# Kernel optimization log

Hardware: AMD Instinct MI355X
Metric: run time of the kernel (lower is better)

Reference implementation:

```python
import jax, jax.numpy as jnp
import numpy as np

UNITS = 512
OUT_STEPS = 32
FEAT = 12  # Dense(12) output fed back as LSTM input


def _lstm_cell(x_t, h, c, W, U, b):
    # Keras LSTMCell gate order: i, f, c(bar), o
    z = x_t @ W + h @ U + b                     # [B, 4U]
    i, f, g, o = jnp.split(z, 4, axis=-1)
    i = jax.nn.sigmoid(i)
    f = jax.nn.sigmoid(f)
    g = jnp.tanh(g)
    o = jax.nn.sigmoid(o)
    c_new = f * c + i * g
    h_new = o * jnp.tanh(c_new)
    return h_new, c_new


def setup_inputs() -> dict:
    key = jax.random.key(0)
    ks = jax.random.split(key, 6)
    B, T = 4096, 128
    s_in = 1.0 / np.sqrt(FEAT)
    s_rec = 1.0 / np.sqrt(UNITS)
    return {
        "x":  jax.random.normal(ks[0], (B, T, FEAT), dtype=jnp.float32),
        "W":  jax.random.normal(ks[1], (FEAT, 4 * UNITS), dtype=jnp.float32) * s_in,
        "U":  jax.random.normal(ks[2], (UNITS, 4 * UNITS), dtype=jnp.float32) * s_rec,
        "b":  jnp.zeros((4 * UNITS,), dtype=jnp.float32),
        "Wd": jax.random.normal(ks[4], (UNITS, FEAT), dtype=jnp.float32) * s_rec,
        "bd": jnp.zeros((FEAT,), dtype=jnp.float32),
    }


def reference(x, W, U, b, Wd, bd):
    B = x.shape[0]
    h0 = jnp.zeros((B, UNITS), dtype=x.dtype)
    c0 = jnp.zeros((B, UNITS), dtype=x.dtype)

    # warmup: run LSTM over full input sequence, keep final state
    def warm_step(carry, x_t):
        h, c = carry
        h, c = _lstm_cell(x_t, h, c, W, U, b)
        return (h, c), None

    (h, c), _ = jax.lax.scan(warm_step, (h0, c0), jnp.swapaxes(x, 0, 1))
    pred0 = h @ Wd + bd                          # [B, 12]

    def ar_step(carry, _):
        h, c, pred = carry
        h, c = _lstm_cell(pred, h, c, W, U, b)
        pred = h @ Wd + bd
        return (h, c, pred), pred

    _, preds_rest = jax.lax.scan(ar_step, (h, c, pred0), None, length=OUT_STEPS - 1)
    preds = jnp.concatenate([pred0[None], preds_rest], axis=0)  # [out_steps, B, 12]
    return jnp.transpose(preds, (1, 0, 2))       # [B, out_steps, 12]
```

## Files before the change

kernel.cpp:

```cpp
#include <hip/hip_runtime.h>


typedef __bf16 bf16;
typedef __attribute__((ext_vector_type(8))) __bf16 bf16x8;
typedef __attribute__((ext_vector_type(4))) float f32x4;

#define NB    4096
#define TSEQ  128
#define FEAT  12
#define UNITS 512
#define NZ    2048
#define OUTS  32

#define BM 128
#define BK 64

#define OFF_UT   ((size_t)0)
#define OFF_UTA  (OFF_UT  + (size_t)NZ*UNITS*2)
#define OFF_WT   (OFF_UTA + (size_t)NZ*UNITS*2)
#define OFF_B2   (OFF_WT  + (size_t)NZ*32*2)
#define OFF_WDT  (OFF_B2  + (size_t)NZ*4)
#define OFF_H0   (OFF_WDT + (size_t)16*UNITS*2)
#define OFF_H1   (OFF_H0  + (size_t)NB*UNITS*2)
#define OFF_C    (OFF_H1  + (size_t)NB*UNITS*2)
#define WS_NEED  (OFF_C   + (size_t)NB*UNITS*4)
#define OFF_HALL (WS_NEED)
#define HALL_SL  ((size_t)NB*UNITS)
#define WS_BIG   (OFF_HALL + (size_t)OUTS*NB*UNITS*2)

__device__ __forceinline__ float fast_exp2(float x){ return __builtin_amdgcn_exp2f(x); }
__device__ __forceinline__ float fast_rcp (float x){ return __builtin_amdgcn_rcpf(x); }
__device__ __forceinline__ float sigm_(float x){ return fast_rcp(1.f + fast_exp2(-1.4426950408889634f*x)); }
__device__ __forceinline__ float tanh_(float x){ return 1.f - 2.f*fast_rcp(1.f + fast_exp2(2.8853900817779268f*x)); }

__global__ void prep_u_kernel(const float* __restrict__ U, const float* __restrict__ W,
                              const float* __restrict__ Wd,
                              bf16* __restrict__ Ut, bf16* __restrict__ Uta){
  __shared__ float su[64][65];
  __shared__ float sa[64][65];
  const int n0 = blockIdx.x * 64;
  const int k0 = blockIdx.y * 64;
  const int tx = threadIdx.x & 63;
  const int rr = threadIdx.x >> 6;
  #pragma unroll 4
  for (int it = 0; it < 16; ++it){
    int k = it*4 + rr;
    float u = U[(size_t)(k0+k)*NZ + n0 + tx];
    float a = u;
    #pragma unroll
    for (int j = 0; j < FEAT; ++j) a += Wd[(k0+k)*FEAT + j] * W[(size_t)j*NZ + n0 + tx];
    su[tx][k] = u;
    sa[tx][k] = a;
  }
  __syncthreads();
  #pragma unroll 4
  for (int it = 0; it < 16; ++it){
    int nl = it*4 + rr;
    Ut [(size_t)(n0+nl)*UNITS + k0 + tx] = (bf16)su[nl][tx];
    Uta[(size_t)(n0+nl)*UNITS + k0 + tx] = (bf16)sa[nl][tx];
  }
}

__global__ void prep_w_kernel(const float* __restrict__ W, const float* __restrict__ b,
                              const float* __restrict__ bd, const float* __restrict__ Wd,
                              bf16* __restrict__ Wt, float* __restrict__ b2,
                              bf16* __restrict__ Wdt){
  const int n = blockIdx.x*256 + threadIdx.x;
  float acc = b[n];
  #pragma unroll
  for (int j = 0; j < FEAT; ++j){
    float w = W[(size_t)j*NZ + n];
    Wt[(size_t)n*32 + j] = (bf16)w;
    acc += bd[j] * w;
  }
  #pragma unroll
  for (int j = FEAT; j < 32; ++j) Wt[(size_t)n*32 + j] = (bf16)0.f;
  b2[n] = acc;
  if (n < UNITS){
    #pragma unroll
    for (int j = 0; j < FEAT; ++j) Wdt[(size_t)j*UNITS + n] = (bf16)Wd[(size_t)n*FEAT + j];
    #pragma unroll
    for (int j = FEAT; j < 16; ++j) Wdt[(size_t)j*UNITS + n] = (bf16)0.f;
  }
}

template<int HAS_X>
__launch_bounds__(256, 2)
__global__ void lstm_step_kernel(const bf16* __restrict__ hin, bf16* __restrict__ hout,
                                 float* __restrict__ c,
                                 const bf16* __restrict__ Bt,
                                 const float* __restrict__ bias,
                                 const float* __restrict__ xt,
                                 const bf16* __restrict__ Wt)
{
  __shared__ alignas(16) char lds[65536];

  int bid = blockIdx.x;
  bid = (bid & 7) * 64 + (bid >> 3);
  const int mt = bid >> 4;
  const int nu = bid & 15;
  const int m0 = mt * BM;

  const int tid  = threadIdx.x;
  const int lane = tid & 63;
  const int wid  = tid >> 6;
  const int wm   = wid >> 1, wn = wid & 1;
  const int l15  = lane & 15;
  const int kgrp = lane >> 4;
  const int l7   = lane & 7;
  const int l8   = lane >> 3;

  const bf16* agp = hin + (size_t)(m0 + wid*32 + l8)*UNITS + l7*8;
  const int   aoff = (wid*32 + l8)*128 + ((l7 ^ l8) << 4);
  int zcv[4];
  #pragma unroll
  for (int i = 0; i < 4; ++i){
    int lnl = wid*32 + i*8 + l8;
    zcv[i] = ((lnl & 3) << 9) + nu*32 + (lnl >> 2);
  }

  f32x4 acc[4][4];
  #pragma unroll
  for (int i = 0; i < 4; ++i)
    #pragma unroll
    for (int j = 0; j < 4; ++j) acc[i][j] = f32x4{0.f,0.f,0.f,0.f};

  bf16x8 rA[2][4], rB[2][4];

  auto load_set = [&](int s, int k0){
    #pragma unroll
    for (int i = 0; i < 4; ++i){
      rA[s][i] = *reinterpret_cast<const bf16x8*>(agp + (size_t)i*8*UNITS + k0);
      rB[s][i] = *reinterpret_cast<const bf16x8*>(Bt + (size_t)zcv[i]*UNITS + k0 + l7*8);
    }
  };
  auto write_set = [&](int s, int bi){
    char* A = lds + (bi << 14);
    char* B = lds + 32768 + (bi << 14);
    #pragma unroll
    for (int i = 0; i < 4; ++i){
      *reinterpret_cast<bf16x8*>(A + aoff + i*1024) = rA[s][i];
      *reinterpret_cast<bf16x8*>(B + aoff + i*1024) = rB[s][i];
    }
  };
  auto compute = [&](int bi){
    const char* A = lds + (bi << 14);
    const char* B = lds + 32768 + (bi << 14);
    #pragma unroll
    for (int kk = 0; kk < 2; ++kk){
      const int sa = (((kk*4 + kgrp) ^ (l15 & 7)) << 4);
      bf16x8 af[4], bq[4];
      #pragma unroll
      for (int f = 0; f < 4; ++f){
        af[f] = *reinterpret_cast<const bf16x8*>(A + (wm*64 + f*16 + l15)*128 + sa);
        bq[f] = *reinterpret_cast<const bf16x8*>(B + (wn*64 + f*16 + l15)*128 + sa);
      }
      #pragma unroll
      for (int i = 0; i < 4; ++i)
        #pragma unroll
        for (int j = 0; j < 4; ++j)
          acc[i][j] = __builtin_amdgcn_mfma_f32_16x16x32_bf16(af[i], bq[j], acc[i][j], 0, 0, 0);
    }
  };

  bf16x8 xa[4], wq[4];
  if (HAS_X){
    #pragma unroll
    for (int f = 0; f < 4; ++f){
      int row = m0 + wm*64 + f*16 + l15;
      const float* xr = xt + (size_t)row * (TSEQ*FEAT);
      bf16x8 v;
      #pragma unroll
      for (int j = 0; j < 8; ++j) v[j] = (bf16)0.f;
      if (kgrp == 0){
        float4 a = *reinterpret_cast<const float4*>(xr);
        float4 b = *reinterpret_cast<const float4*>(xr + 4);
        v[0]=(bf16)a.x; v[1]=(bf16)a.y; v[2]=(bf16)a.z; v[3]=(bf16)a.w;
        v[4]=(bf16)b.x; v[5]=(bf16)b.y; v[6]=(bf16)b.z; v[7]=(bf16)b.w;
      } else if (kgrp == 1){
        float4 a = *reinterpret_cast<const float4*>(xr + 8);
        v[0]=(bf16)a.x; v[1]=(bf16)a.y; v[2]=(bf16)a.z; v[3]=(bf16)a.w;
      }
      xa[f] = v;
      int lnl = wn*64 + f*16 + l15;
      int zc  = ((lnl & 3) << 9) + nu*32 + (lnl >> 2);
      wq[f] = *reinterpret_cast<const bf16x8*>(Wt + (size_t)zc*32 + kgrp*8);
    }
  }
  const int eu  = tid & 31;
  const int erg = tid >> 5;
  const int cu  = nu*32 + eu;
  float bi_ = bias[0*UNITS + cu];
  float bf_ = bias[1*UNITS + cu];
  float bg_ = bias[2*UNITS + cu];
  float bo_ = bias[3*UNITS + cu];

  load_set(0, 0);
  load_set(1, BK);

  const int rbase = m0 + erg*16;
  float cold[16];
  {
    const float* cp = c + (size_t)rbase*UNITS + cu;
    #pragma unroll
    for (int r = 0; r < 16; ++r) cold[r] = cp[(size_t)r*UNITS];
  }

  write_set(0, 0);
  asm volatile("s_waitcnt lgkmcnt(0)" ::: "memory");
  __builtin_amdgcn_sched_barrier(0);
  __builtin_amdgcn_s_barrier();

  #pragma unroll
  for (int t = 0; t < 8; ++t){
    const int p = t & 1;
    if (t + 2 < 8) load_set(p, (t+2)*BK);
    compute(p);
    if (t < 7){
      write_set(p ^ 1, p ^ 1);
      asm volatile("s_waitcnt lgkmcnt(0)" ::: "memory");
      __builtin_amdgcn_sched_barrier(0);
      __builtin_amdgcn_s_barrier();
    }
  }

  if (HAS_X){
    #pragma unroll
    for (int i = 0; i < 4; ++i)
      #pragma unroll
      for (int j = 0; j < 4; ++j)
        acc[i][j] = __builtin_amdgcn_mfma_f32_16x16x32_bf16(xa[i], wq[j], acc[i][j], 0, 0, 0);
  }

  asm volatile("s_waitcnt lgkmcnt(0)" ::: "memory");
  __builtin_amdgcn_sched_barrier(0);
  __builtin_amdgcn_s_barrier();

  #pragma unroll
  for (int fm = 0; fm < 4; ++fm){
    #pragma unroll
    for (int fn = 0; fn < 4; ++fn){
      int col  = wn*64 + fn*16 + l15;
      int srow = wm*16 + fm*4 + kgrp;
      *reinterpret_cast<f32x4*>(lds + col*512 + ((srow ^ (col & 7)) << 4)) = acc[fm][fn];
    }
  }
  asm volatile("s_waitcnt lgkmcnt(0)" ::: "memory");
  __builtin_amdgcn_sched_barrier(0);
  __builtin_amdgcn_s_barrier();

  #pragma unroll
  for (int q = 0; q < 4; ++q){
    const int s = erg*4 + q;
    f32x4 zi = *reinterpret_cast<const f32x4*>(lds + (eu*4+0)*512 + ((s ^ ((eu*4+0)&7)) << 4));
    f32x4 zf = *reinterpret_cast<const f32x4*>(lds + (eu*4+1)*512 + ((s ^ ((eu*4+1)&7)) << 4));
    f32x4 zg = *reinterpret_cast<const f32x4*>(lds + (eu*4+2)*512 + ((s ^ ((eu*4+2)&7)) << 4));
    f32x4 zo = *reinterpret_cast<const f32x4*>(lds + (eu*4+3)*512 + ((s ^ ((eu*4+3)&7)) << 4));
    #pragma unroll
    for (int rr = 0; rr < 4; ++rr){
      int r = q*4 + rr;
      float iv = sigm_(zi[rr] + bi_);
      float fv = sigm_(zf[rr] + bf_);
      float gv = tanh_(zg[rr] + bg_);
      float ov = sigm_(zo[rr] + bo_);
      float cn = fv*cold[r] + iv*gv;
      size_t idx = (size_t)(rbase + r)*UNITS + cu;
      c[idx]    = cn;
      hout[idx] = (bf16)(ov*tanh_(cn));
    }
  }
}

__global__ void pred_all_kernel(const bf16* __restrict__ hbase, size_t slot_stride, int s0,
                                const bf16* __restrict__ Wdt,
                                const float* __restrict__ bd, float* __restrict__ out){
  const int slot = s0 + blockIdx.y;
  const bf16* h  = hbase + (size_t)blockIdx.y * slot_stride;
  const int tid = threadIdx.x, lane = tid & 63, wid = tid >> 6;
  const int l15 = lane & 15, kg = lane >> 4;
  const int r0 = blockIdx.x*64 + wid*16;
  f32x4 acc = f32x4{0.f,0.f,0.f,0.f};
  const bf16* ap = h   + (size_t)(r0 + l15)*UNITS + kg*8;
  const bf16* bp = Wdt + (size_t)l15*UNITS + kg*8;
  #pragma unroll
  for (int ks = 0; ks < 16; ++ks){
    bf16x8 a = *reinterpret_cast<const bf16x8*>(ap + ks*32);
    bf16x8 b = *reinterpret_cast<const bf16x8*>(bp + ks*32);
    acc = __builtin_amdgcn_mfma_f32_16x16x32_bf16(a, b, acc, 0, 0, 0);
  }
  if (l15 < FEAT){
    float bdv = bd[l15];
    #pragma unroll
    for (int r = 0; r < 4; ++r){
      int row = r0 + kg*4 + r;
      out[(size_t)row*(OUTS*FEAT) + slot*FEAT + l15] = acc[r] + bdv;
    }
  }
}

extern "C" void kernel_launch(void* const* d_in, const int* in_sizes, int n_in,
                              void* d_out, int out_size, void* d_ws, size_t ws_size,
                              hipStream_t stream){
  const float* x  = (const float*)d_in[0];
  const float* W  = (const float*)d_in[1];
  const float* U  = (const float*)d_in[2];
  const float* b  = (const float*)d_in[3];
  const float* Wd = (const float*)d_in[4];
  const float* bd = (const float*)d_in[5];
  float* out = (float*)d_out;
  (void)in_sizes; (void)n_in; (void)out_size;
  if (ws_size < WS_NEED) return;
  const bool big = ws_size >= WS_BIG;

  char* ws  = (char*)d_ws;
  bf16* Ut  = (bf16*)(ws + OFF_UT);
  bf16* Uta = (bf16*)(ws + OFF_UTA);
  bf16* Wt  = (bf16*)(ws + OFF_WT);
  float* b2 = (float*)(ws + OFF_B2);
  bf16* Wdt = (bf16*)(ws + OFF_WDT);
  bf16* h0  = (bf16*)(ws + OFF_H0);
  bf16* h1  = (bf16*)(ws + OFF_H1);
  float* c  = (float*)(ws + OFF_C);
  bf16* hall= (bf16*)(ws + OFF_HALL);

  hipMemsetAsync(h0, 0, (size_t)NB*UNITS*2, stream);
  hipMemsetAsync(c,  0, (size_t)NB*UNITS*4, stream);
  prep_u_kernel<<<dim3(32, 8), 256, 0, stream>>>(U, W, Wd, Ut, Uta);
  prep_w_kernel<<<8, 256, 0, stream>>>(W, b, bd, Wd, Wt, b2, Wdt);

  if (big){
    bf16* hcur = h0; bf16* hnxt = h1;
    for (int t = 0; t < TSEQ; ++t){
      bf16* dst = (t == TSEQ-1) ? hall : hnxt;
      lstm_step_kernel<1><<<512, 256, 0, stream>>>(hcur, dst, c, Ut, b, x + t*FEAT, Wt);
      hnxt = hcur; hcur = dst;
    }
    for (int s = 1; s < OUTS; ++s)
      lstm_step_kernel<0><<<512, 256, 0, stream>>>(hall + (size_t)(s-1)*HALL_SL,
                                                   hall + (size_t)s*HALL_SL,
                                                   c, Uta, b2, nullptr, nullptr);
    pred_all_kernel<<<dim3(NB/64, OUTS), 256, 0, stream>>>(hall, HALL_SL, 0, Wdt, bd, out);
  } else {
    bf16* hcur = h0; bf16* hnxt = h1;
    for (int t = 0; t < TSEQ; ++t){
      lstm_step_kernel<1><<<512, 256, 0, stream>>>(hcur, hnxt, c, Ut, b, x + t*FEAT, Wt);
      bf16* tmp = hcur; hcur = hnxt; hnxt = tmp;
    }
    pred_all_kernel<<<dim3(NB/64, 1), 256, 0, stream>>>(hcur, 0, 0, Wdt, bd, out);
    for (int s = 1; s < OUTS; ++s){
      lstm_step_kernel<0><<<512, 256, 0, stream>>>(hcur, hnxt, c, Uta, b2, nullptr, nullptr);
      bf16* tmp = hcur; hcur = hnxt; hnxt = tmp;
      pred_all_kernel<<<dim3(NB/64, 1), 256, 0, stream>>>(hcur, 0, s, Wdt, bd, out);
    }
  }
}
```

Baseline: 2.950 ms.

## Replace per-step launches with persistent cooperative LSTM kernel using row-tile barriers

Runs all 159 recurrent steps inside one cooperative persistent kernel of 512 blocks. Each block keeps its cell state in registers instead of reading and writing c in global memory every step. Steps are synchronized with a per-row-tile atomic counter barrier rather than kernel boundaries, so only the 16 blocks sharing a batch tile wait on each other. This removes launch overhead and the c round-trip, but relies on all blocks being co-resident and adds spin-wait latency. If the cooperative launch fails, it falls back to the old multi-launch path.

```diff
diff --git a/kernel.cpp b/kernel.cpp
--- a/kernel.cpp
+++ b/kernel.cpp
@@ -11,6 +11,7 @@
 #define UNITS 512
 #define NZ    2048
 #define OUTS  32
+#define NSTEP (TSEQ + OUTS - 1)
 
 #define BM 128
 #define BK 64
@@ -23,7 +24,8 @@
 #define OFF_H0   (OFF_WDT + (size_t)16*UNITS*2)
 #define OFF_H1   (OFF_H0  + (size_t)NB*UNITS*2)
 #define OFF_C    (OFF_H1  + (size_t)NB*UNITS*2)
-#define WS_NEED  (OFF_C   + (size_t)NB*UNITS*4)
+#define OFF_BAR  (OFF_C   + (size_t)NB*UNITS*4)
+#define WS_NEED  (OFF_BAR + 4096)
 #define OFF_HALL (WS_NEED)
 #define HALL_SL  ((size_t)NB*UNITS)
 #define WS_BIG   (OFF_HALL + (size_t)OUTS*NB*UNITS*2)
@@ -84,6 +86,226 @@
   }
 }
 
+__launch_bounds__(256, 2)
+__global__ void lstm_persistent(bf16* __restrict__ hA,
+                                bf16* __restrict__ hB,
+                                bf16* __restrict__ hall,
+                                const bf16* __restrict__ Ut,
+                                const bf16* __restrict__ Uta,
+                                const float* __restrict__ b1,
+                                const float* __restrict__ b2,
+                                const float* __restrict__ x,
+                                const bf16* __restrict__ Wt,
+                                unsigned* __restrict__ bar)
+{
+  __shared__ alignas(16) char lds[65536];
+
+  int bid = blockIdx.x;
+  bid = (bid & 7) * 64 + (bid >> 3);
+  const int mt = bid >> 4;
+  const int nu = bid & 15;
+  const int m0 = mt * BM;
+
+  const int tid  = threadIdx.x;
+  const int lane = tid & 63;
+  const int wid  = tid >> 6;
+  const int wm   = wid >> 1, wn = wid & 1;
+  const int l15  = lane & 15;
+  const int kgrp = lane >> 4;
+  const int l7   = lane & 7;
+  const int l8   = lane >> 3;
+
+  const int    aoff = (wid*32 + l8)*128 + ((l7 ^ l8) << 4);
+  const size_t arow = (size_t)(m0 + wid*32 + l8)*UNITS + l7*8;
+  int zcv[4];
+  #pragma unroll
+  for (int i = 0; i < 4; ++i){
+    int lnl = wid*32 + i*8 + l8;
+    zcv[i] = ((lnl & 3) << 9) + nu*32 + (lnl >> 2);
+  }
+
+  bf16x8 wq[4];
+  int    xrow[4];
+  #pragma unroll
+  for (int f = 0; f < 4; ++f){
+    int lnl = wn*64 + f*16 + l15;
+    int zc  = ((lnl & 3) << 9) + nu*32 + (lnl >> 2);
+    wq[f] = *reinterpret_cast<const bf16x8*>(Wt + (size_t)zc*32 + kgrp*8);
+    xrow[f] = (m0 + wm*64 + f*16 + l15) * (TSEQ*FEAT);
+  }
+  const int eu  = tid & 31;
+  const int erg = tid >> 5;
+  const int cu  = nu*32 + eu;
+  const float bI1 = b1[0*UNITS+cu], bF1 = b1[1*UNITS+cu], bG1 = b1[2*UNITS+cu], bO1 = b1[3*UNITS+cu];
+  const float bI2 = b2[0*UNITS+cu], bF2 = b2[1*UNITS+cu], bG2 = b2[2*UNITS+cu], bO2 = b2[3*UNITS+cu];
+  const int rbase = m0 + erg*16;
+
+  float cc[16];
+  #pragma unroll
+  for (int r = 0; r < 16; ++r) cc[r] = 0.f;
+
+  f32x4 acc[4][4];
+  bf16x8 rA[2][4], rB[2][4];
+
+  #pragma unroll 1
+  for (int t = 0; t < NSTEP; ++t){
+    const bool hasx = (t < TSEQ);
+    const bf16* Bt = hasx ? Ut : Uta;
+    const bf16* hi = (t < TSEQ) ? ((t & 1) ? hB : hA)
+                                : hall + (size_t)(t - TSEQ)*HALL_SL;
+    bf16* ho = (t < TSEQ-1) ? ((t & 1) ? hA : hB)
+                            : hall + (size_t)(t - (TSEQ-1))*HALL_SL;
+
+    bf16x8 xa[4];
+    if (hasx){
+      #pragma unroll
+      for (int f = 0; f < 4; ++f){
+        const float* xr = x + xrow[f] + t*FEAT;
+        bf16x8 v;
+        #pragma unroll
+        for (int j = 0; j < 8; ++j) v[j] = (bf16)0.f;
+        if (kgrp == 0){
+          float4 a = *reinterpret_cast<const float4*>(xr);
+          float4 b = *reinterpret_cast<const float4*>(xr + 4);
+          v[0]=(bf16)a.x; v[1]=(bf16)a.y; v[2]=(bf16)a.z; v[3]=(bf16)a.w;
+          v[4]=(bf16)b.x; v[5]=(bf16)b.y; v[6]=(bf16)b.z; v[7]=(bf16)b.w;
+        } else if (kgrp == 1){
+          float4 a = *reinterpret_cast<const float4*>(xr + 8);
+          v[0]=(bf16)a.x; v[1]=(bf16)a.y; v[2]=(bf16)a.z; v[3]=(bf16)a.w;
+        }
+        xa[f] = v;
+      }
+    }
+
+    if (t > 0){
+      if (tid == 0){
+        const unsigned tgt = 16u * (unsigned)t;
+        while (__hip_atomic_load(&bar[mt], __ATOMIC_RELAXED, __HIP_MEMORY_SCOPE_AGENT) < tgt)
+          __builtin_amdgcn_s_sleep(4);
+        __builtin_amdgcn_fence(__ATOMIC_ACQUIRE, "agent");
+      }
+      __syncthreads();
+    }
+
+    auto load_set = [&](int s, int k0){
+      #pragma unroll
+      for (int i = 0; i < 4; ++i){
+        rA[s][i] = *reinterpret_cast<const bf16x8*>(hi + arow + (size_t)i*8*UNITS + k0);
+        rB[s][i] = *reinterpret_cast<const bf16x8*>(Bt + (size_t)zcv[i]*UNITS + k0 + l7*8);
+      }
+    };
+    auto write_set = [&](int s, int bi){
+      char* A = lds + (bi << 14);
+      char* B = lds + 32768 + (bi << 14);
+      #pragma unroll
+      for (int i = 0; i < 4; ++i){
+        *reinterpret_cast<bf16x8*>(A + aoff + i*1024) = rA[s][i];
+        *reinterpret_cast<bf16x8*>(B + aoff + i*1024) = rB[s][i];
+      }
+    };
+    auto compute = [&](int bi){
+      const char* A = lds + (bi << 14);
+      const char* B = lds + 32768 + (bi << 14);
+      #pragma unroll
+      for (int kk = 0; kk < 2; ++kk){
+        const int sa = (((kk*4 + kgrp) ^ (l15 & 7)) << 4);
+        bf16x8 af[4], bq[4];
+        #pragma unroll
+        for (int f = 0; f < 4; ++f){
+          af[f] = *reinterpret_cast<const bf16x8*>(A + (wm*64 + f*16 + l15)*128 + sa);
+          bq[f] = *reinterpret_cast<const bf16x8*>(B + (wn*64 + f*16 + l15)*128 + sa);
+        }
+        #pragma unroll
+        for (int i = 0; i < 4; ++i)
+          #pragma unroll
+          for (int j = 0; j < 4; ++j)
+            acc[i][j] = __builtin_amdgcn_mfma_f32_16x16x32_bf16(af[i], bq[j], acc[i][j], 0, 0, 0);
+      }
+    };
+
+    #pragma unroll
+    for (int i = 0; i < 4; ++i)
+      #pragma unroll
+      for (int j = 0; j < 4; ++j) acc[i][j] = f32x4{0.f,0.f,0.f,0.f};
+
+    load_set(0, 0);
+    load_set(1, BK);
+    write_set(0, 0);
+    asm volatile("s_waitcnt lgkmcnt(0)" ::: "memory");
+    __builtin_amdgcn_sched_barrier(0);
+    __builtin_amdgcn_s_barrier();
+
+    #pragma unroll
+    for (int kt = 0; kt < 8; ++kt){
+      const int p = kt & 1;
+      if (kt + 2 < 8) load_set(p, (kt+2)*BK);
+      compute(p);
+      if (kt < 7){
+        write_set(p ^ 1, p ^ 1);
+        asm volatile("s_waitcnt lgkmcnt(0)" ::: "memory");
+        __builtin_amdgcn_sched_barrier(0);
+        __builtin_amdgcn_s_barrier();
+      }
+    }
+
+    if (hasx){
+      #pragma unroll
+      for (int i = 0; i < 4; ++i)
+        #pragma unroll
+        for (int j = 0; j < 4; ++j)
+          acc[i][j] = __builtin_amdgcn_mfma_f32_16x16x32_bf16(xa[i], wq[j], acc[i][j], 0, 0, 0);
+    }
+
+    asm volatile("s_waitcnt lgkmcnt(0)" ::: "memory");
+    __builtin_amdgcn_sched_barrier(0);
+    __builtin_amdgcn_s_barrier();
+
+    #pragma unroll
+    for (int fm = 0; fm < 4; ++fm){
+      #pragma unroll
+      for (int fn = 0; fn < 4; ++fn){
+        int col  = wn*64 + fn*16 + l15;
+        int srow = wm*16 + fm*4 + kgrp;
+        *reinterpret_cast<f32x4*>(lds + col*512 + ((srow ^ (col & 7)) << 4)) = acc[fm][fn];
+      }
+    }
+    asm volatile("s_waitcnt lgkmcnt(0)" ::: "memory");
+    __builtin_amdgcn_sched_barrier(0);
+    __builtin_amdgcn_s_barrier();
+
+    const float bi_ = hasx ? bI1 : bI2;
+    const float bf_ = hasx ? bF1 : bF2;
+    const float bg_ = hasx ? bG1 : bG2;
+    const float bo_ = hasx ? bO1 : bO2;
+
+    #pragma unroll
+    for (int q = 0; q < 4; ++q){
+      const int s = erg*4 + q;
+      f32x4 zi = *reinterpret_cast<const f32x4*>(lds + (eu*4+0)*512 + ((s ^ ((eu*4+0)&7)) << 4));
+      f32x4 zf = *reinterpret_cast<const f32x4*>(lds + (eu*4+1)*512 + ((s ^ ((eu*4+1)&7)) << 4));
+      f32x4 zg = *reinterpret_cast<const f32x4*>(lds + (eu*4+2)*512 + ((s ^ ((eu*4+2)&7)) << 4));
+      f32x4 zo = *reinterpret_cast<const f32x4*>(lds + (eu*4+3)*512 + ((s ^ ((eu*4+3)&7)) << 4));
+      #pragma unroll
+      for (int rr2 = 0; rr2 < 4; ++rr2){
+        int r = q*4 + rr2;
+        float iv = sigm_(zi[rr2] + bi_);
+        float fv = sigm_(zf[rr2] + bf_);
+        float gv = tanh_(zg[rr2] + bg_);
+        float ov = sigm_(zo[rr2] + bo_);
+        float cn = fv*cc[r] + iv*gv;
+        cc[r] = cn;
+        ho[(size_t)(rbase + r)*UNITS + cu] = (bf16)(ov*tanh_(cn));
+      }
+    }
+
+    if (t < NSTEP - 1){
+      __syncthreads();
+      if (tid == 0)
+        __hip_atomic_fetch_add(&bar[mt], 1u, __ATOMIC_RELEASE, __HIP_MEMORY_SCOPE_AGENT);
+    }
+  }
+}
+
 template<int HAS_X>
 __launch_bounds__(256, 2)
 __global__ void lstm_step_kernel(const bf16* __restrict__ hin, bf16* __restrict__ hout,
@@ -94,13 +316,11 @@
                                  const bf16* __restrict__ Wt)
 {
   __shared__ alignas(16) char lds[65536];
-
   int bid = blockIdx.x;
   bid = (bid & 7) * 64 + (bid >> 3);
   const int mt = bid >> 4;
   const int nu = bid & 15;
   const int m0 = mt * BM;
-
   const int tid  = threadIdx.x;
   const int lane = tid & 63;
   const int wid  = tid >> 6;
@@ -126,7 +346,6 @@
     for (int j = 0; j < 4; ++j) acc[i][j] = f32x4{0.f,0.f,0.f,0.f};
 
   bf16x8 rA[2][4], rB[2][4];
-
   auto load_set = [&](int s, int k0){
     #pragma unroll
     for (int i = 0; i < 4; ++i){
@@ -197,7 +416,6 @@
 
   load_set(0, 0);
   load_set(1, BK);
-
   const int rbase = m0 + erg*16;
   float cold[16];
   {
@@ -205,7 +423,6 @@
     #pragma unroll
     for (int r = 0; r < 16; ++r) cold[r] = cp[(size_t)r*UNITS];
   }
-
   write_set(0, 0);
   asm volatile("s_waitcnt lgkmcnt(0)" ::: "memory");
   __builtin_amdgcn_sched_barrier(0);
@@ -235,7 +452,6 @@
   asm volatile("s_waitcnt lgkmcnt(0)" ::: "memory");
   __builtin_amdgcn_sched_barrier(0);
   __builtin_amdgcn_s_barrier();
-
   #pragma unroll
   for (int fm = 0; fm < 4; ++fm){
     #pragma unroll
@@ -321,36 +537,55 @@
   bf16* h0  = (bf16*)(ws + OFF_H0);
   bf16* h1  = (bf16*)(ws + OFF_H1);
   float* c  = (float*)(ws + OFF_C);
+  unsigned* bar = (unsigned*)(ws + OFF_BAR);
   bf16* hall= (bf16*)(ws + OFF_HALL);
 
   hipMemsetAsync(h0, 0, (size_t)NB*UNITS*2, stream);
   hipMemsetAsync(c,  0, (size_t)NB*UNITS*4, stream);
+  hipMemsetAsync(bar, 0, 4096, stream);
   prep_u_kernel<<<dim3(32, 8), 256, 0, stream>>>(U, W, Wd, Ut, Uta);
   prep_w_kernel<<<8, 256, 0, stream>>>(W, b, bd, Wd, Wt, b2, Wdt);
 
+  bool done = false;
   if (big){
-    bf16* hcur = h0; bf16* hnxt = h1;
-    for (int t = 0; t < TSEQ; ++t){
-      bf16* dst = (t == TSEQ-1) ? hall : hnxt;
-      lstm_step_kernel<1><<<512, 256, 0, stream>>>(hcur, dst, c, Ut, b, x + t*FEAT, Wt);
-      hnxt = hcur; hcur = dst;
-    }
-    for (int s = 1; s < OUTS; ++s)
-      lstm_step_kernel<0><<<512, 256, 0, stream>>>(hall + (size_t)(s-1)*HALL_SL,
-                                                   hall + (size_t)s*HALL_SL,
-                                                   c, Uta, b2, nullptr, nullptr);
-    pred_all_kernel<<<dim3(NB/64, OUTS), 256, 0, stream>>>(hall, HALL_SL, 0, Wdt, bd, out);
-  } else {
-    bf16* hcur = h0; bf16* hnxt = h1;
-    for (int t = 0; t < TSEQ; ++t){
-      lstm_step_kernel<1><<<512, 256, 0, stream>>>(hcur, hnxt, c, Ut, b, x + t*FEAT, Wt);
-      bf16* tmp = hcur; hcur = hnxt; hnxt = tmp;
-    }
-    pred_all_kernel<<<dim3(NB/64, 1), 256, 0, stream>>>(hcur, 0, 0, Wdt, bd, out);
-    for (int s = 1; s < OUTS; ++s){
-      lstm_step_kernel<0><<<512, 256, 0, stream>>>(hcur, hnxt, c, Uta, b2, nullptr, nullptr);
-      bf16* tmp = hcur; hcur = hnxt; hnxt = tmp;
-      pred_all_kernel<<<dim3(NB/64, 1), 256, 0, stream>>>(hcur, 0, s, Wdt, bd, out);
+    const float* xc = x;
+    void* args[] = { (void*)&h0, (void*)&h1, (void*)&hall,
+                     (void*)&Ut, (void*)&Uta, (void*)&b, (void*)&b2,
+                     (void*)&xc, (void*)&Wt, (void*)&bar };
+    hipError_t e = hipLaunchCooperativeKernel(
+        reinterpret_cast<void*>(lstm_persistent),
+        dim3(512), dim3(256), args, 0, stream);
+    if (e == hipSuccess){
+      pred_all_kernel<<<dim3(NB/64, OUTS), 256, 0, stream>>>(hall, HALL_SL, 0, Wdt, bd, out);
+      done = true;
+    }
+  }
+
+  if (!done){
+    if (big){
+      bf16* hcur = h0; bf16* hnxt = h1;
+      for (int t = 0; t < TSEQ; ++t){
+        bf16* dst = (t == TSEQ-1) ? hall : hnxt;
+        lstm_step_kernel<1><<<512, 256, 0, stream>>>(hcur, dst, c, Ut, b, x + t*FEAT, Wt);
+        hnxt = hcur; hcur = dst;
+      }
+      for (int s = 1; s < OUTS; ++s)
+        lstm_step_kernel<0><<<512, 256, 0, stream>>>(hall + (size_t)(s-1)*HALL_SL,
+                                                     hall + (size_t)s*HALL_SL,
+                                                     c, Uta, b2, nullptr, nullptr);
+      pred_all_kernel<<<dim3(NB/64, OUTS), 256, 0, stream>>>(hall, HALL_SL, 0, Wdt, bd, out);
+    } else {
+      bf16* hcur = h0; bf16* hnxt = h1;
+      for (int t = 0; t < TSEQ; ++t){
+        lstm_step_kernel<1><<<512, 256, 0, stream>>>(hcur, hnxt, c, Ut, b, x + t*FEAT, Wt);
+        bf16* tmp = hcur; hcur = hnxt; hnxt = tmp;
+      }
+      pred_all_kernel<<<dim3(NB/64, 1), 256, 0, stream>>>(hcur, 0, 0, Wdt, bd, out);
+      for (int s = 1; s < OUTS; ++s){
+        lstm_step_kernel<0><<<512, 256, 0, stream>>>(hcur, hnxt, c, Uta, b2, nullptr, nullptr);
+        bf16* tmp = hcur; hcur = hnxt; hnxt = tmp;
+        pred_all_kernel<<<dim3(NB/64, 1), 256, 0, stream>>>(hcur, 0, s, Wdt, bd, out);
+      }
     }
   }
 }
```

Measured after the change: 5.886 ms. +99.6%, slower.

## Pre-pack recurrent weights into MFMA fragment order and load B directly to registers

Applied to the files above, without the earlier changes.

The prep kernel now writes the transposed U and U+Wd·W matrices in a packed layout that matches each wave's MFMA B-fragment order. The step kernel loads B fragments straight from global memory into registers instead of staging them through LDS, so only the A (hidden state) tile goes through shared memory. This cuts LDS writes and reads for B and the bank traffic they cause. In exchange it needs more registers for the doubled B prefetch buffers, which may pressure occupancy under the 2-waves-per-SIMD launch bound, and each wave now fetches its own B data from global memory or L2.

```diff
diff --git a/kernel.cpp b/kernel.cpp
--- a/kernel.cpp
+++ b/kernel.cpp
@@ -33,9 +33,20 @@
 __device__ __forceinline__ float sigm_(float x){ return fast_rcp(1.f + fast_exp2(-1.4426950408889634f*x)); }
 __device__ __forceinline__ float tanh_(float x){ return 1.f - 2.f*fast_rcp(1.f + fast_exp2(2.8853900817779268f*x)); }
 
+__device__ __forceinline__ size_t bp_off(int n, int k){
+  int g  = n >> 9;
+  int uc = n & 511;
+  int nu = uc >> 5, uo = uc & 31;
+  int lnl = uo*4 + g;
+  int wn = lnl >> 6, f = (lnl >> 4) & 3, l15 = lnl & 15;
+  int it = k >> 6, kk = (k >> 5) & 1, kgrp = (k >> 3) & 3, e = k & 7;
+  int frag = (((nu*2 + wn)*4 + f)*8 + it)*2 + kk;
+  return (size_t)frag*1024 + kgrp*256 + l15*16 + e*2;
+}
+
 __global__ void prep_u_kernel(const float* __restrict__ U, const float* __restrict__ W,
                               const float* __restrict__ Wd,
-                              bf16* __restrict__ Ut, bf16* __restrict__ Uta){
+                              bf16* __restrict__ Utp, bf16* __restrict__ Utap){
   __shared__ float su[64][65];
   __shared__ float sa[64][65];
   const int n0 = blockIdx.x * 64;
@@ -53,11 +64,17 @@
     sa[tx][k] = a;
   }
   __syncthreads();
-  #pragma unroll 4
-  for (int it = 0; it < 16; ++it){
-    int nl = it*4 + rr;
-    Ut [(size_t)(n0+nl)*UNITS + k0 + tx] = (bf16)su[nl][tx];
-    Uta[(size_t)(n0+nl)*UNITS + k0 + tx] = (bf16)sa[nl][tx];
+  const int nl = threadIdx.x & 63;
+  const int q  = threadIdx.x >> 6;
+  const float (*src)[65] = (q & 1) ? sa : su;
+  char* dst = (char*)((q & 1) ? Utap : Utp);
+  const int kh = (q >> 1) * 32;
+  #pragma unroll
+  for (int kc = 0; kc < 32; kc += 8){
+    bf16x8 v;
+    #pragma unroll
+    for (int e = 0; e < 8; ++e) v[e] = (bf16)src[nl][kh + kc + e];
+    *reinterpret_cast<bf16x8*>(dst + bp_off(n0 + nl, k0 + kh + kc)) = v;
   }
 }
 
@@ -88,7 +105,7 @@
 __launch_bounds__(256, 2)
 __global__ void lstm_step_kernel(const bf16* __restrict__ hin, bf16* __restrict__ hout,
                                  float* __restrict__ c,
-                                 const bf16* __restrict__ Bt,
+                                 const bf16* __restrict__ Bp,
                                  const float* __restrict__ bias,
                                  const float* __restrict__ xt,
                                  const bf16* __restrict__ Wt)
@@ -112,12 +129,8 @@
 
   const bf16* agp = hin + (size_t)(m0 + wid*32 + l8)*UNITS + l7*8;
   const int   aoff = (wid*32 + l8)*128 + ((l7 ^ l8) << 4);
-  int zcv[4];
-  #pragma unroll
-  for (int i = 0; i < 4; ++i){
-    int lnl = wid*32 + i*8 + l8;
-    zcv[i] = ((lnl & 3) << 9) + nu*32 + (lnl >> 2);
-  }
+
+  const char* bp = (const char*)Bp + (size_t)(nu*2 + wn)*65536 + kgrp*256 + l15*16;
 
   f32x4 acc[4][4];
   #pragma unroll
@@ -125,41 +138,41 @@
     #pragma unroll
     for (int j = 0; j < 4; ++j) acc[i][j] = f32x4{0.f,0.f,0.f,0.f};
 
-  bf16x8 rA[2][4], rB[2][4];
-
-  auto load_set = [&](int s, int k0){
-    #pragma unroll
-    for (int i = 0; i < 4; ++i){
+  bf16x8 rA[2][4];
+  bf16x8 rB[2][8];
+
+  auto loadA_set = [&](int s, int k0){
+    #pragma unroll
+    for (int i = 0; i < 4; ++i)
       rA[s][i] = *reinterpret_cast<const bf16x8*>(agp + (size_t)i*8*UNITS + k0);
-      rB[s][i] = *reinterpret_cast<const bf16x8*>(Bt + (size_t)zcv[i]*UNITS + k0 + l7*8);
-    }
   };
-  auto write_set = [&](int s, int bi){
+  auto loadB_set = [&](int s, int it){
+    #pragma unroll
+    for (int f = 0; f < 4; ++f)
+      #pragma unroll
+      for (int kk = 0; kk < 2; ++kk)
+        rB[s][f*2+kk] = *reinterpret_cast<const bf16x8*>(bp + f*16384 + it*2048 + kk*1024);
+  };
+  auto writeA_set = [&](int s, int bi){
     char* A = lds + (bi << 14);
-    char* B = lds + 32768 + (bi << 14);
-    #pragma unroll
-    for (int i = 0; i < 4; ++i){
+    #pragma unroll
+    for (int i = 0; i < 4; ++i)
       *reinterpret_cast<bf16x8*>(A + aoff + i*1024) = rA[s][i];
-      *reinterpret_cast<bf16x8*>(B + aoff + i*1024) = rB[s][i];
-    }
   };
-  auto compute = [&](int bi){
+  auto compute = [&](int bi, int s){
     const char* A = lds + (bi << 14);
-    const char* B = lds + 32768 + (bi << 14);
     #pragma unroll
     for (int kk = 0; kk < 2; ++kk){
       const int sa = (((kk*4 + kgrp) ^ (l15 & 7)) << 4);
-      bf16x8 af[4], bq[4];
-      #pragma unroll
-      for (int f = 0; f < 4; ++f){
+      bf16x8 af[4];
+      #pragma unroll
+      for (int f = 0; f < 4; ++f)
         af[f] = *reinterpret_cast<const bf16x8*>(A + (wm*64 + f*16 + l15)*128 + sa);
-        bq[f] = *reinterpret_cast<const bf16x8*>(B + (wn*64 + f*16 + l15)*128 + sa);
-      }
       #pragma unroll
       for (int i = 0; i < 4; ++i)
         #pragma unroll
         for (int j = 0; j < 4; ++j)
-          acc[i][j] = __builtin_amdgcn_mfma_f32_16x16x32_bf16(af[i], bq[j], acc[i][j], 0, 0, 0);
+          acc[i][j] = __builtin_amdgcn_mfma_f32_16x16x32_bf16(af[i], rB[s][j*2+kk], acc[i][j], 0, 0, 0);
     }
   };
 
@@ -195,8 +208,10 @@
   float bg_ = bias[2*UNITS + cu];
   float bo_ = bias[3*UNITS + cu];
 
-  load_set(0, 0);
-  load_set(1, BK);
+  loadA_set(0, 0);
+  loadB_set(0, 0);
+  loadA_set(1, BK);
+  loadB_set(1, 1);
 
   const int rbase = m0 + erg*16;
   float cold[16];
@@ -206,7 +221,7 @@
     for (int r = 0; r < 16; ++r) cold[r] = cp[(size_t)r*UNITS];
   }
 
-  write_set(0, 0);
+  writeA_set(0, 0);
   asm volatile("s_waitcnt lgkmcnt(0)" ::: "memory");
   __builtin_amdgcn_sched_barrier(0);
   __builtin_amdgcn_s_barrier();
@@ -214,10 +229,11 @@
   #pragma unroll
   for (int t = 0; t < 8; ++t){
     const int p = t & 1;
-    if (t + 2 < 8) load_set(p, (t+2)*BK);
-    compute(p);
+    if (t + 2 < 8) loadA_set(p, (t+2)*BK);
+    compute(p, p);
+    if (t + 2 < 8) loadB_set(p, t+2);
     if (t < 7){
-      write_set(p ^ 1, p ^ 1);
+      writeA_set(p ^ 1, p ^ 1);
       asm volatile("s_waitcnt lgkmcnt(0)" ::: "memory");
       __builtin_amdgcn_sched_barrier(0);
       __builtin_amdgcn_s_barrier();
@@ -313,8 +329,8 @@
   const bool big = ws_size >= WS_BIG;
 
   char* ws  = (char*)d_ws;
-  bf16* Ut  = (bf16*)(ws + OFF_UT);
-  bf16* Uta = (bf16*)(ws + OFF_UTA);
+  bf16* Utp = (bf16*)(ws + OFF_UT);
+  bf16* Utap= (bf16*)(ws + OFF_UTA);
   bf16* Wt  = (bf16*)(ws + OFF_WT);
   float* b2 = (float*)(ws + OFF_B2);
   bf16* Wdt = (bf16*)(ws + OFF_WDT);
@@ -325,30 +341,30 @@
 
   hipMemsetAsync(h0, 0, (size_t)NB*UNITS*2, stream);
   hipMemsetAsync(c,  0, (size_t)NB*UNITS*4, stream);
-  prep_u_kernel<<<dim3(32, 8), 256, 0, stream>>>(U, W, Wd, Ut, Uta);
+  prep_u_kernel<<<dim3(32, 8), 256, 0, stream>>>(U, W, Wd, Utp, Utap);
   prep_w_kernel<<<8, 256, 0, stream>>>(W, b, bd, Wd, Wt, b2, Wdt);
 
   if (big){
     bf16* hcur = h0; bf16* hnxt = h1;
     for (int t = 0; t < TSEQ; ++t){
       bf16* dst = (t == TSEQ-1) ? hall : hnxt;
-      lstm_step_kernel<1><<<512, 256, 0, stream>>>(hcur, dst, c, Ut, b, x + t*FEAT, Wt);
+      lstm_step_kernel<1><<<512, 256, 0, stream>>>(hcur, dst, c, Utp, b, x + t*FEAT, Wt);
       hnxt = hcur; hcur = dst;
     }
     for (int s = 1; s < OUTS; ++s)
       lstm_step_kernel<0><<<512, 256, 0, stream>>>(hall + (size_t)(s-1)*HALL_SL,
                                                    hall + (size_t)s*HALL_SL,
-                                                   c, Uta, b2, nullptr, nullptr);
+                                                   c, Utap, b2, nullptr, nullptr);
     pred_all_kernel<<<dim3(NB/64, OUTS), 256, 0, stream>>>(hall, HALL_SL, 0, Wdt, bd, out);
   } else {
     bf16* hcur = h0; bf16* hnxt = h1;
     for (int t = 0; t < TSEQ; ++t){
-      lstm_step_kernel<1><<<512, 256, 0, stream>>>(hcur, hnxt, c, Ut, b, x + t*FEAT, Wt);
+      lstm_step_kernel<1><<<512, 256, 0, stream>>>(hcur, hnxt, c, Utp, b, x + t*FEAT, Wt);
       bf16* tmp = hcur; hcur = hnxt; hnxt = tmp;
     }
     pred_all_kernel<<<dim3(NB/64, 1), 256, 0, stream>>>(hcur, 0, 0, Wdt, bd, out);
     for (int s = 1; s < OUTS; ++s){
-      lstm_step_kernel<0><<<512, 256, 0, stream>>>(hcur, hnxt, c, Uta, b2, nullptr, nullptr);
+      lstm_step_kernel<0><<<512, 256, 0, stream>>>(hcur, hnxt, c, Utap, b2, nullptr, nullptr);
       bf16* tmp = hcur; hcur = hnxt; hnxt = tmp;
       pred_all_kernel<<<dim3(NB/64, 1), 256, 0, stream>>>(hcur, 0, s, Wdt, bd, out);
     }
```

Result: slower. 3.157 ms (+7.0%).
